# Kernel optimization log

Measured on AMD Instinct MI355X. Metric: run time of the kernel, lower is better.

## Reference

```python
import jax, jax.numpy as jnp
import numpy as np

B, S, H, NH, P = 1, 2048, 1024, 16, 2
D = H // NH
SCALE = 1.0 / np.sqrt(D).astype(np.float32)


def _lin(x, W, b):
    # x: [..., in] @ W: [in, out] + b: [out]
    return x @ W + b


def _split_heads(x):
    # [..., S, H] -> [..., NH, S, D]
    return x.reshape(*x.shape[:-2], x.shape[-2], NH, D).swapaxes(-3, -2)


def _merge_heads(x):
    # [..., NH, S, D] -> [..., S, H]
    return x.swapaxes(-3, -2).reshape(*x.shape[:-3], x.shape[-2], H)


def setup_inputs() -> dict:
    key = jax.random.key(0)
    ks = jax.random.split(key, 20)
    w = lambda k, i, o: jax.random.normal(k, (i, o), jnp.float32) * 0.02
    inp = {
        "hidden_states": jax.random.normal(ks[0], (B, S, H), jnp.float32),
        "past_states": jax.random.normal(ks[1], (P, B, S, H), jnp.float32),
        "Wq": w(ks[2], H, H), "bq": jnp.zeros((H,), jnp.float32),
        "Wk": w(ks[3], H, H), "bk": jnp.zeros((H,), jnp.float32),
        "Wv": w(ks[4], H, H), "bv": jnp.zeros((H,), jnp.float32),
        "Wo": w(ks[5], H, H), "bo": jnp.zeros((H,), jnp.float32),
        "Wrq": w(ks[6], H, H), "brq": jnp.zeros((H,), jnp.float32),
        "Wrk": w(ks[7], H, H), "brk": jnp.zeros((H,), jnp.float32),
        "Wrv": w(ks[8], H, H), "brv": jnp.zeros((H,), jnp.float32),
        "Wg": w(ks[9], 2 * H, H), "bg": jnp.zeros((H,), jnp.float32),
    }
    return inp


def reference(hidden_states, past_states, Wq, bq, Wk, bk, Wv, bv, Wo, bo,
              Wrq, brq, Wrk, brk, Wrv, brv, Wg, bg):
    # --- standard self-attention ---
    q = _split_heads(_lin(hidden_states, Wq, bq))  # [B,NH,S,D]
    k = _split_heads(_lin(hidden_states, Wk, bk))
    v = _split_heads(_lin(hidden_states, Wv, bv))
    scores = jnp.einsum('bhsd,bhtd->bhst', q, k) * SCALE
    attn = jax.nn.softmax(scores, axis=-1)
    ctx = jnp.einsum('bhst,bhtd->bhsd', attn, v)
    output = _lin(_merge_heads(ctx), Wo, bo)  # [B,S,H]

    # --- recursive attention over past states (recursion_level > 0) ---
    rq = _split_heads(_lin(output, Wrq, brq))           # [B,NH,S,D]
    rk = _split_heads(_lin(past_states, Wrk, brk))      # [P,B,NH,S,D]
    rv = _split_heads(_lin(past_states, Wrv, brv))
    rscores = jnp.einsum('bhsd,pbhtd->pbhst', rq, rk) * SCALE
    rattn = jax.nn.softmax(rscores, axis=-1)
    rctx = jnp.einsum('pbhst,pbhtd->pbhsd', rattn, rv)
    recursive_output = _merge_heads(rctx).mean(axis=0)  # [B,S,H]

    gate = jax.nn.sigmoid(_lin(jnp.concatenate([output, recursive_output], axis=-1), Wg, bg))
    output = output * (1.0 - gate) + recursive_output * gate
    return output
```

## Files before the change

### kernel.cpp

```cpp
#include <hip/hip_runtime.h>
#include <hip/hip_bf16.h>

#define S_LEN 2048
#define HDIM  1024
#define NHEAD 16
#define DHEAD 64
#define SCALE_F 0.125f
#define QSCALE  (0.125f * 1.44269504088896340736f)

typedef __bf16 bf16;
typedef __bf16 bf16x4 __attribute__((ext_vector_type(4)));
typedef __bf16 bf16x8 __attribute__((ext_vector_type(8)));
typedef float  f32x4  __attribute__((ext_vector_type(4)));

#define MFMA16(a,b,c) __builtin_amdgcn_mfma_f32_16x16x32_bf16((a),(b),(c),0,0,0)

__device__ __forceinline__ void gload16(const bf16* g, bf16* lds_wave_base) {
  __builtin_amdgcn_global_load_lds(
      (const __attribute__((address_space(1))) void*)g,
      (__attribute__((address_space(3))) void*)lds_wave_base, 16, 0, 0);
}

__global__ void cvt_f32_bf16_kernel(const float* __restrict__ in,
                                    bf16* __restrict__ out, int n4) {
  int i = blockIdx.x * blockDim.x + threadIdx.x;
  int stride = gridDim.x * blockDim.x;
  for (; i < n4; i += stride) {
    float4 v = ((const float4*)in)[i];
    bf16x4 o = { (bf16)v.x, (bf16)v.y, (bf16)v.z, (bf16)v.w };
    ((bf16x4*)out)[i] = o;
  }
}

struct TrJob { const float* in; bf16* out; };
struct TrArgs { TrJob j[8]; };

__global__ void transp_cvt_kernel(TrArgs args, int rows, int cols) {
  TrJob t = args.j[blockIdx.z];
  __shared__ float tile[32][33];
  int tx = threadIdx.x, ty = threadIdx.y;
  int c0 = blockIdx.x * 32, r0 = blockIdx.y * 32;
  for (int j = ty; j < 32; j += 8)
    tile[j][tx] = t.in[(size_t)(r0 + j) * cols + c0 + tx];
  __syncthreads();
  for (int j = ty; j < 32; j += 8)
    t.out[(size_t)(c0 + j) * rows + r0 + tx] = (bf16)tile[tx][j];
}

__global__ void transp_head_kernel(const bf16* __restrict__ in,
                                   bf16* __restrict__ out) {
  __shared__ bf16 tile[32][33];
  int h = blockIdx.z;
  int t0 = blockIdx.x * 32, d0 = blockIdx.y * 32;
  int tx = threadIdx.x, ty = threadIdx.y;
  for (int j = ty; j < 32; j += 8)
    tile[j][tx] = in[(size_t)(t0 + j) * HDIM + h * DHEAD + d0 + tx];
  __syncthreads();
  for (int j = ty; j < 32; j += 8)
    out[((size_t)h * DHEAD + d0 + j) * S_LEN + t0 + tx] = tile[tx][j];
}

struct GemmJob { const bf16* A; const bf16* Bt; const float* bias; bf16* Cb; float* Cf; float cscale; };
struct GemmArgs { GemmJob j[6]; };

__launch_bounds__(256)
__global__ void gemm_bt_kernel(GemmArgs args, int M, int N, int K) {
  GemmJob jb = args.j[blockIdx.z];
  const int bn = blockIdx.x, bm = blockIdx.y;
  const int tid = threadIdx.x;
  const int wave = tid >> 6, lane = tid & 63;
  const int wr = wave >> 1, wc = wave & 1;
  const int l16 = lane & 15, lq = lane >> 4;

  __shared__ alignas(16) bf16 As[128 * 32];
  __shared__ alignas(16) bf16 Bs[128 * 32];

  f32x4 acc[4][4];
#pragma unroll
  for (int i = 0; i < 4; ++i)
#pragma unroll
    for (int j = 0; j < 4; ++j) acc[i][j] = (f32x4){0.f, 0.f, 0.f, 0.f};

  const bf16* Ap = jb.A + (size_t)bm * 128 * K;
  const bf16* Bp = jb.Bt + (size_t)bn * 128 * K;

  const int r0 = tid >> 2,           c0 = (tid & 3) << 3;
  const int r1 = (tid + 256) >> 2,   c1 = ((tid + 256) & 3) << 3;
  bf16* ldsA0 = As + wave * 512;
  bf16* ldsA1 = As + 2048 + wave * 512;
  bf16* ldsB0 = Bs + wave * 512;
  bf16* ldsB1 = Bs + 2048 + wave * 512;

  for (int kt = 0; kt < K; kt += 32) {
    __syncthreads();
    gload16(Ap + (size_t)r0 * K + kt + c0, ldsA0);
    gload16(Ap + (size_t)r1 * K + kt + c1, ldsA1);
    gload16(Bp + (size_t)r0 * K + kt + c0, ldsB0);
    gload16(Bp + (size_t)r1 * K + kt + c1, ldsB1);
    __syncthreads();

    bf16x8 af[4], bfr[4];
#pragma unroll
    for (int i = 0; i < 4; ++i)
      af[i] = *(const bf16x8*)(As + (size_t)(wr * 64 + i * 16 + l16) * 32 + lq * 8);
#pragma unroll
    for (int j = 0; j < 4; ++j)
      bfr[j] = *(const bf16x8*)(Bs + (size_t)(wc * 64 + j * 16 + l16) * 32 + lq * 8);
#pragma unroll
    for (int i = 0; i < 4; ++i)
#pragma unroll
      for (int j = 0; j < 4; ++j)
        acc[i][j] = MFMA16(af[i], bfr[j], acc[i][j]);
  }

#pragma unroll
  for (int i = 0; i < 4; ++i) {
#pragma unroll
    for (int j = 0; j < 4; ++j) {
      int row0 = bm * 128 + wr * 64 + i * 16 + lq * 4;
      int col  = bn * 128 + wc * 64 + j * 16 + l16;
      float bv = jb.bias ? jb.bias[col] : 0.0f;
#pragma unroll
      for (int r = 0; r < 4; ++r) {
        float v = (acc[i][j][r] + bv) * jb.cscale;
        size_t off = (size_t)(row0 + r) * N + col;
        if (jb.Cb) jb.Cb[off] = (bf16)v;
        if (jb.Cf) jb.Cf[off] = v;
      }
    }
  }
}

__launch_bounds__(256)
__global__ void flash_attn_kernel(const bf16* __restrict__ Q,
                                  const bf16* __restrict__ Kin,
                                  const bf16* __restrict__ VT,
                                  bf16* __restrict__ Ob,
                                  float* __restrict__ Of,
                                  size_t kStride, size_t vStride, size_t oStride) {
  const int qb = blockIdx.x, h = blockIdx.y, p = blockIdx.z;
  const bf16* Kp = Kin + (size_t)p * kStride;
  const bf16* Vp = VT + (size_t)p * vStride;
  const int tid = threadIdx.x;
  const int wave = tid >> 6, lane = tid & 63;
  const int l16 = lane & 15, lq = lane >> 4;

  __shared__ alignas(16) bf16 Ks[64][72];
  __shared__ alignas(16) bf16 Vs[64][72];
  __shared__ alignas(16) bf16 Ps[4][16][72];

  bf16x8 qf[2];
  {
    const bf16* qptr = Q + (size_t)(qb * 64 + wave * 16 + l16) * HDIM + h * DHEAD + lq * 8;
    qf[0] = *(const bf16x8*)qptr;
    qf[1] = *(const bf16x8*)(qptr + 32);
  }

  float m_run = -1e30f, l_run = 0.f;
  f32x4 oacc[4];
#pragma unroll
  for (int j = 0; j < 4; ++j) oacc[j] = (f32x4){0.f, 0.f, 0.f, 0.f};

  for (int tb = 0; tb < S_LEN / 64; ++tb) {
    __syncthreads();
#pragma unroll
    for (int it = 0; it < 2; ++it) {
      int idx = tid + it * 256;
      int r = idx >> 3, c8 = (idx & 7) << 3;
      *(bf16x8*)(&Ks[r][c8]) = *(const bf16x8*)(Kp + (size_t)(tb * 64 + r) * HDIM + h * DHEAD + c8);
      *(bf16x8*)(&Vs[r][c8]) = *(const bf16x8*)(Vp + ((size_t)h * DHEAD + r) * S_LEN + tb * 64 + c8);
    }
    __syncthreads();

    f32x4 sf[4];
#pragma unroll
    for (int j = 0; j < 4; ++j) sf[j] = (f32x4){0.f, 0.f, 0.f, 0.f};
#pragma unroll
    for (int j = 0; j < 4; ++j)
#pragma unroll
      for (int kk = 0; kk < 2; ++kk) {
        bf16x8 kf = *(const bf16x8*)(&Ks[j * 16 + l16][kk * 32 + lq * 8]);
        sf[j] = MFMA16(kf, qf[kk], sf[j]);
      }

    float mx = -1e30f;
#pragma unroll
    for (int j = 0; j < 4; ++j)
#pragma unroll
      for (int r = 0; r < 4; ++r) mx = fmaxf(mx, sf[j][r]);
    mx = fmaxf(mx, __shfl_xor(mx, 16));
    mx = fmaxf(mx, __shfl_xor(mx, 32));

    float mnew = fmaxf(m_run, mx);
    float corr = exp2f(m_run - mnew);
    m_run = mnew;

    float rs = 0.f;
#pragma unroll
    for (int j = 0; j < 4; ++j)
#pragma unroll
      for (int r = 0; r < 4; ++r) {
        float pv = exp2f(sf[j][r] - mnew);
        sf[j][r] = pv;
        rs += pv;
      }
    rs += __shfl_xor(rs, 16);
    rs += __shfl_xor(rs, 32);
    l_run = l_run * corr + rs;
#pragma unroll
    for (int j = 0; j < 4; ++j) {
      oacc[j][0] *= corr; oacc[j][1] *= corr; oacc[j][2] *= corr; oacc[j][3] *= corr;
    }

#pragma unroll
    for (int j = 0; j < 4; ++j) {
      bf16x4 pk = { (bf16)sf[j][0], (bf16)sf[j][1], (bf16)sf[j][2], (bf16)sf[j][3] };
      *(bf16x4*)(&Ps[wave][l16][j * 16 + lq * 4]) = pk;
    }
    asm volatile("s_waitcnt lgkmcnt(0)" ::: "memory");

    bf16x8 pf[2];
    pf[0] = *(const bf16x8*)(&Ps[wave][l16][lq * 8]);
    pf[1] = *(const bf16x8*)(&Ps[wave][l16][32 + lq * 8]);
#pragma unroll
    for (int j = 0; j < 4; ++j)
#pragma unroll
      for (int kk = 0; kk < 2; ++kk) {
        bf16x8 vtf = *(const bf16x8*)(&Vs[j * 16 + l16][kk * 32 + lq * 8]);
        oacc[j] = MFMA16(vtf, pf[kk], oacc[j]);
      }
  }

  const float inv = 1.0f / l_run;
  const int q = qb * 64 + wave * 16 + l16;
#pragma unroll
  for (int j = 0; j < 4; ++j) {
    size_t off = (size_t)q * HDIM + h * DHEAD + j * 16 + lq * 4;
    float o0 = oacc[j][0] * inv, o1 = oacc[j][1] * inv,
          o2 = oacc[j][2] * inv, o3 = oacc[j][3] * inv;
    if (Ob) {
      bf16x4 ov = { (bf16)o0, (bf16)o1, (bf16)o2, (bf16)o3 };
      *(bf16x4*)(Ob + off) = ov;
    }
    if (Of) {
      float4 ov = { o0, o1, o2, o3 };
      *(float4*)(Of + (size_t)p * oStride + off) = ov;
    }
  }
}

__global__ void mean_gate_prep_kernel(const float* __restrict__ rc,
                                      const bf16* __restrict__ outb,
                                      float* __restrict__ rof,
                                      bf16* __restrict__ acat,
                                      int n) {
  int i = blockIdx.x * blockDim.x + threadIdx.x;
  int stride = gridDim.x * blockDim.x;
  for (; i < n; i += stride) {
    float ro = 0.5f * (rc[i] + rc[i + n]);
    rof[i] = ro;
    int srow = i >> 10, col = i & 1023;
    size_t base = (size_t)srow * 2048;
    acat[base + col] = outb[i];
    acat[base + 1024 + col] = (bf16)ro;
  }
}

__global__ void final_gate_kernel(const float* __restrict__ outf,
                                  const float* __restrict__ rof,
                                  const float* __restrict__ glog,
                                  float* __restrict__ out, int n) {
  int i = blockIdx.x * blockDim.x + threadIdx.x;
  int stride = gridDim.x * blockDim.x;
  for (; i < n; i += stride) {
    float g = 1.0f / (1.0f + __expf(-glog[i]));
    out[i] = outf[i] * (1.0f - g) + rof[i] * g;
  }
}

extern "C" void kernel_launch(void* const* d_in, const int* in_sizes, int n_in,
                              void* d_out, int out_size, void* d_ws, size_t ws_size,
                              hipStream_t stream) {
  const float* hs   = (const float*)d_in[0];
  const float* past = (const float*)d_in[1];
  const float* Wq = (const float*)d_in[2];   const float* bq = (const float*)d_in[3];
  const float* Wk = (const float*)d_in[4];   const float* bk = (const float*)d_in[5];
  const float* Wv = (const float*)d_in[6];   const float* bv = (const float*)d_in[7];
  const float* Wo = (const float*)d_in[8];   const float* bo = (const float*)d_in[9];
  const float* Wrq = (const float*)d_in[10]; const float* brq = (const float*)d_in[11];
  const float* Wrk = (const float*)d_in[12]; const float* brk = (const float*)d_in[13];
  const float* Wrv = (const float*)d_in[14]; const float* brv = (const float*)d_in[15];
  const float* Wg  = (const float*)d_in[16]; const float* bg  = (const float*)d_in[17];

  char* wp = (char*)d_ws;
  auto alloc = [&](size_t bytes) -> void* {
    void* p = (void*)wp;
    wp += (bytes + 255) & ~(size_t)255;
    return p;
  };
  const size_t NE = (size_t)S_LEN * HDIM;

  bf16* hs_b   = (bf16*)alloc(NE * 2);
  bf16* past_b = (bf16*)alloc(2 * NE * 2);
  bf16* Wqt  = (bf16*)alloc((size_t)HDIM * HDIM * 2);
  bf16* Wkt  = (bf16*)alloc((size_t)HDIM * HDIM * 2);
  bf16* Wvt  = (bf16*)alloc((size_t)HDIM * HDIM * 2);
  bf16* Wot  = (bf16*)alloc((size_t)HDIM * HDIM * 2);
  bf16* Wrqt = (bf16*)alloc((size_t)HDIM * HDIM * 2);
  bf16* Wrkt = (bf16*)alloc((size_t)HDIM * HDIM * 2);
  bf16* Wrvt = (bf16*)alloc((size_t)HDIM * HDIM * 2);
  bf16* Wgt  = (bf16*)alloc((size_t)2 * HDIM * HDIM * 2);
  bf16* q_b   = (bf16*)alloc(NE * 2);
  bf16* k_b   = (bf16*)alloc(NE * 2);
  bf16* v_b   = (bf16*)alloc(NE * 2);
  bf16* vT_b  = (bf16*)alloc(NE * 2);
  bf16* ctx_b = (bf16*)alloc(NE * 2);
  bf16* out_b = (bf16*)alloc(NE * 2);
  float* out_f = (float*)alloc(NE * 4);
  bf16* rq_b  = (bf16*)alloc(NE * 2);
  bf16* rk_b  = (bf16*)alloc(2 * NE * 2);
  bf16* rv_b  = (bf16*)alloc(2 * NE * 2);
  bf16* rvT_b = (bf16*)alloc(2 * NE * 2);
  float* rctx_f = (float*)alloc(2 * NE * 4);
  float* ro_f   = (float*)alloc(NE * 4);
  bf16* acat_b  = (bf16*)alloc(2 * NE * 2);
  float* glog_f = (float*)alloc(NE * 4);

  cvt_f32_bf16_kernel<<<2048, 256, 0, stream>>>(hs, hs_b, (int)(NE / 4));
  cvt_f32_bf16_kernel<<<2048, 256, 0, stream>>>(past, past_b, (int)(2 * NE / 4));

  TrArgs ta{};
  ta.j[0] = {Wq, Wqt};  ta.j[1] = {Wk, Wkt};  ta.j[2] = {Wv, Wvt};
  ta.j[3] = {Wo, Wot};  ta.j[4] = {Wrq, Wrqt}; ta.j[5] = {Wrk, Wrkt};
  ta.j[6] = {Wrv, Wrvt};
  transp_cvt_kernel<<<dim3(32, 32, 7), dim3(32, 8), 0, stream>>>(ta, 1024, 1024);
  TrArgs tg{};
  tg.j[0] = {Wg, Wgt};
  transp_cvt_kernel<<<dim3(32, 64, 1), dim3(32, 8), 0, stream>>>(tg, 2048, 1024);

  GemmArgs g1{};
  g1.j[0] = {hs_b, Wqt, bq, q_b, nullptr, QSCALE};
  g1.j[1] = {hs_b, Wkt, bk, k_b, nullptr, 1.0f};
  g1.j[2] = {hs_b, Wvt, bv, v_b, nullptr, 1.0f};
  gemm_bt_kernel<<<dim3(8, 16, 3), 256, 0, stream>>>(g1, 2048, 1024, 1024);

  transp_head_kernel<<<dim3(64, 2, 16), dim3(32, 8), 0, stream>>>(v_b, vT_b);

  flash_attn_kernel<<<dim3(32, 16, 1), 256, 0, stream>>>(
      q_b, k_b, vT_b, ctx_b, nullptr, 0, 0, 0);

  GemmArgs g2{};
  g2.j[0] = {ctx_b, Wot, bo, out_b, out_f, 1.0f};
  gemm_bt_kernel<<<dim3(8, 16, 1), 256, 0, stream>>>(g2, 2048, 1024, 1024);

  GemmArgs g3{};
  g3.j[0] = {out_b,        Wrqt, brq, rq_b,      nullptr, QSCALE};
  g3.j[1] = {past_b,       Wrkt, brk, rk_b,      nullptr, 1.0f};
  g3.j[2] = {past_b + NE,  Wrkt, brk, rk_b + NE, nullptr, 1.0f};
  g3.j[3] = {past_b,       Wrvt, brv, rv_b,      nullptr, 1.0f};
  g3.j[4] = {past_b + NE,  Wrvt, brv, rv_b + NE, nullptr, 1.0f};
  gemm_bt_kernel<<<dim3(8, 16, 5), 256, 0, stream>>>(g3, 2048, 1024, 1024);

  transp_head_kernel<<<dim3(64, 2, 16), dim3(32, 8), 0, stream>>>(rv_b, rvT_b);
  transp_head_kernel<<<dim3(64, 2, 16), dim3(32, 8), 0, stream>>>(rv_b + NE, rvT_b + NE);

  flash_attn_kernel<<<dim3(32, 16, 2), 256, 0, stream>>>(
      rq_b, rk_b, rvT_b, nullptr, rctx_f, NE, NE, NE);

  mean_gate_prep_kernel<<<2048, 256, 0, stream>>>(rctx_f, out_b, ro_f, acat_b, (int)NE);

  GemmArgs g4{};
  g4.j[0] = {acat_b, Wgt, bg, nullptr, glog_f, 1.0f};
  gemm_bt_kernel<<<dim3(8, 16, 1), 256, 0, stream>>>(g4, 2048, 1024, 2048);

  final_gate_kernel<<<2048, 256, 0, stream>>>(out_f, ro_f, glog_f, (float*)d_out, (int)NE);
}
```

Measured before the change: 474.6 us.

## Double-buffer GEMM and attention tiles, shrink GEMM M-tile, batch independent projections

Result: faster. 434.5 us (-8.4%).

```diff
diff --git a/kernel.cpp b/kernel.cpp
--- a/kernel.cpp
+++ b/kernel.cpp
@@ -5,7 +5,6 @@
 #define HDIM  1024
 #define NHEAD 16
 #define DHEAD 64
-#define SCALE_F 0.125f
 #define QSCALE  (0.125f * 1.44269504088896340736f)
 
 typedef __bf16 bf16;
@@ -47,21 +46,24 @@
     t.out[(size_t)(c0 + j) * rows + r0 + tx] = (bf16)tile[tx][j];
 }
 
-__global__ void transp_head_kernel(const bf16* __restrict__ in,
-                                   bf16* __restrict__ out) {
+struct ThJob { const bf16* in; bf16* out; };
+struct ThArgs { ThJob j[4]; };
+
+__global__ void transp_head_kernel(ThArgs args) {
+  ThJob t = args.j[blockIdx.z >> 4];
+  int h = blockIdx.z & 15;
   __shared__ bf16 tile[32][33];
-  int h = blockIdx.z;
   int t0 = blockIdx.x * 32, d0 = blockIdx.y * 32;
   int tx = threadIdx.x, ty = threadIdx.y;
   for (int j = ty; j < 32; j += 8)
-    tile[j][tx] = in[(size_t)(t0 + j) * HDIM + h * DHEAD + d0 + tx];
+    tile[j][tx] = t.in[(size_t)(t0 + j) * HDIM + h * DHEAD + d0 + tx];
   __syncthreads();
   for (int j = ty; j < 32; j += 8)
-    out[((size_t)h * DHEAD + d0 + j) * S_LEN + t0 + tx] = tile[tx][j];
+    t.out[((size_t)h * DHEAD + d0 + j) * S_LEN + t0 + tx] = tile[tx][j];
 }
 
 struct GemmJob { const bf16* A; const bf16* Bt; const float* bias; bf16* Cb; float* Cf; float cscale; };
-struct GemmArgs { GemmJob j[6]; };
+struct GemmArgs { GemmJob j[8]; };
 
 __launch_bounds__(256)
 __global__ void gemm_bt_kernel(GemmArgs args, int M, int N, int K) {
@@ -72,52 +74,57 @@
   const int wr = wave >> 1, wc = wave & 1;
   const int l16 = lane & 15, lq = lane >> 4;
 
-  __shared__ alignas(16) bf16 As[128 * 32];
-  __shared__ alignas(16) bf16 Bs[128 * 32];
-
-  f32x4 acc[4][4];
-#pragma unroll
-  for (int i = 0; i < 4; ++i)
+  __shared__ alignas(16) bf16 As[2][64 * 32];
+  __shared__ alignas(16) bf16 Bs[2][128 * 32];
+
+  f32x4 acc[2][4];
+#pragma unroll
+  for (int i = 0; i < 2; ++i)
 #pragma unroll
     for (int j = 0; j < 4; ++j) acc[i][j] = (f32x4){0.f, 0.f, 0.f, 0.f};
 
-  const bf16* Ap = jb.A + (size_t)bm * 128 * K;
+  const bf16* Ap = jb.A + (size_t)bm * 64 * K;
   const bf16* Bp = jb.Bt + (size_t)bn * 128 * K;
 
-  const int r0 = tid >> 2,           c0 = (tid & 3) << 3;
-  const int r1 = (tid + 256) >> 2,   c1 = ((tid + 256) & 3) << 3;
-  bf16* ldsA0 = As + wave * 512;
-  bf16* ldsA1 = As + 2048 + wave * 512;
-  bf16* ldsB0 = Bs + wave * 512;
-  bf16* ldsB1 = Bs + 2048 + wave * 512;
-
-  for (int kt = 0; kt < K; kt += 32) {
-    __syncthreads();
-    gload16(Ap + (size_t)r0 * K + kt + c0, ldsA0);
-    gload16(Ap + (size_t)r1 * K + kt + c1, ldsA1);
-    gload16(Bp + (size_t)r0 * K + kt + c0, ldsB0);
-    gload16(Bp + (size_t)r1 * K + kt + c1, ldsB1);
-    __syncthreads();
-
-    bf16x8 af[4], bfr[4];
-#pragma unroll
-    for (int i = 0; i < 4; ++i)
-      af[i] = *(const bf16x8*)(As + (size_t)(wr * 64 + i * 16 + l16) * 32 + lq * 8);
+  const int c0 = wave * 64 + lane;
+  const int r0 = c0 >> 2, c08 = (c0 & 3) << 3;
+
+  auto STAGE = [&](int buf, int kt) {
+    gload16(Ap + (size_t)r0 * K + kt + c08, &As[buf][wave * 512]);
+    gload16(Bp + (size_t)r0 * K + kt + c08, &Bs[buf][wave * 512]);
+    gload16(Bp + (size_t)(r0 + 64) * K + kt + c08, &Bs[buf][2048 + wave * 512]);
+  };
+
+  const int NT = K >> 5;
+  STAGE(0, 0);
+  __syncthreads();
+
+  for (int t = 0; t < NT; ++t) {
+    const int cur = t & 1;
+    const int ktn = (t + 1 < NT) ? (t + 1) * 32 : t * 32;
+    STAGE(cur ^ 1, ktn);
+
+    bf16x8 af[2], bfr[4];
+#pragma unroll
+    for (int i = 0; i < 2; ++i)
+      af[i] = *(const bf16x8*)(&As[cur][(wr * 32 + i * 16 + l16) * 32 + lq * 8]);
 #pragma unroll
     for (int j = 0; j < 4; ++j)
-      bfr[j] = *(const bf16x8*)(Bs + (size_t)(wc * 64 + j * 16 + l16) * 32 + lq * 8);
-#pragma unroll
-    for (int i = 0; i < 4; ++i)
+      bfr[j] = *(const bf16x8*)(&Bs[cur][(wc * 64 + j * 16 + l16) * 32 + lq * 8]);
+#pragma unroll
+    for (int i = 0; i < 2; ++i)
 #pragma unroll
       for (int j = 0; j < 4; ++j)
         acc[i][j] = MFMA16(af[i], bfr[j], acc[i][j]);
-  }
-
-#pragma unroll
-  for (int i = 0; i < 4; ++i) {
+
+    __syncthreads();
+  }
+
+#pragma unroll
+  for (int i = 0; i < 2; ++i) {
 #pragma unroll
     for (int j = 0; j < 4; ++j) {
-      int row0 = bm * 128 + wr * 64 + i * 16 + lq * 4;
+      int row0 = bm * 64 + wr * 32 + i * 16 + lq * 4;
       int col  = bn * 128 + wc * 64 + j * 16 + l16;
       float bv = jb.bias ? jb.bias[col] : 0.0f;
 #pragma unroll
@@ -145,9 +152,27 @@
   const int wave = tid >> 6, lane = tid & 63;
   const int l16 = lane & 15, lq = lane >> 4;
 
-  __shared__ alignas(16) bf16 Ks[64][72];
-  __shared__ alignas(16) bf16 Vs[64][72];
+  __shared__ alignas(16) bf16 Ks[2][64][72];
+  __shared__ alignas(16) bf16 Vs[2][64][72];
   __shared__ alignas(16) bf16 Ps[4][16][72];
+
+  const int i0 = tid, i1 = tid + 256;
+  const int ra = i0 >> 3, ca = (i0 & 7) << 3;
+  const int rb = i1 >> 3, cb = (i1 & 7) << 3;
+
+  bf16x8 krg[2], vrg[2];
+  auto LOAD_TILE = [&](int tb) {
+    krg[0] = *(const bf16x8*)(Kp + (size_t)(tb * 64 + ra) * HDIM + h * DHEAD + ca);
+    krg[1] = *(const bf16x8*)(Kp + (size_t)(tb * 64 + rb) * HDIM + h * DHEAD + cb);
+    vrg[0] = *(const bf16x8*)(Vp + ((size_t)h * DHEAD + ra) * S_LEN + tb * 64 + ca);
+    vrg[1] = *(const bf16x8*)(Vp + ((size_t)h * DHEAD + rb) * S_LEN + tb * 64 + cb);
+  };
+  auto STORE_TILE = [&](int buf) {
+    *(bf16x8*)(&Ks[buf][ra][ca]) = krg[0];
+    *(bf16x8*)(&Ks[buf][rb][cb]) = krg[1];
+    *(bf16x8*)(&Vs[buf][ra][ca]) = vrg[0];
+    *(bf16x8*)(&Vs[buf][rb][cb]) = vrg[1];
+  };
 
   bf16x8 qf[2];
   {
@@ -161,16 +186,15 @@
 #pragma unroll
   for (int j = 0; j < 4; ++j) oacc[j] = (f32x4){0.f, 0.f, 0.f, 0.f};
 
-  for (int tb = 0; tb < S_LEN / 64; ++tb) {
-    __syncthreads();
-#pragma unroll
-    for (int it = 0; it < 2; ++it) {
-      int idx = tid + it * 256;
-      int r = idx >> 3, c8 = (idx & 7) << 3;
-      *(bf16x8*)(&Ks[r][c8]) = *(const bf16x8*)(Kp + (size_t)(tb * 64 + r) * HDIM + h * DHEAD + c8);
-      *(bf16x8*)(&Vs[r][c8]) = *(const bf16x8*)(Vp + ((size_t)h * DHEAD + r) * S_LEN + tb * 64 + c8);
-    }
-    __syncthreads();
+  const int NT = S_LEN / 64;
+  LOAD_TILE(0);
+  STORE_TILE(0);
+  __syncthreads();
+
+  for (int tb = 0; tb < NT; ++tb) {
+    const int cur = tb & 1;
+    const bool more = (tb + 1 < NT);
+    if (more) LOAD_TILE(tb + 1);
 
     f32x4 sf[4];
 #pragma unroll
@@ -179,7 +203,7 @@
     for (int j = 0; j < 4; ++j)
 #pragma unroll
       for (int kk = 0; kk < 2; ++kk) {
-        bf16x8 kf = *(const bf16x8*)(&Ks[j * 16 + l16][kk * 32 + lq * 8]);
+        bf16x8 kf = *(const bf16x8*)(&Ks[cur][j * 16 + l16][kk * 32 + lq * 8]);
         sf[j] = MFMA16(kf, qf[kk], sf[j]);
       }
 
@@ -226,9 +250,14 @@
     for (int j = 0; j < 4; ++j)
 #pragma unroll
       for (int kk = 0; kk < 2; ++kk) {
-        bf16x8 vtf = *(const bf16x8*)(&Vs[j * 16 + l16][kk * 32 + lq * 8]);
+        bf16x8 vtf = *(const bf16x8*)(&Vs[cur][j * 16 + l16][kk * 32 + lq * 8]);
         oacc[j] = MFMA16(vtf, pf[kk], oacc[j]);
       }
+
+    if (more) {
+      STORE_TILE(cur ^ 1);
+      __syncthreads();
+    }
   }
 
   const float inv = 1.0f / l_run;
@@ -339,30 +368,31 @@
   transp_cvt_kernel<<<dim3(32, 64, 1), dim3(32, 8), 0, stream>>>(tg, 2048, 1024);
 
   GemmArgs g1{};
-  g1.j[0] = {hs_b, Wqt, bq, q_b, nullptr, QSCALE};
-  g1.j[1] = {hs_b, Wkt, bk, k_b, nullptr, 1.0f};
-  g1.j[2] = {hs_b, Wvt, bv, v_b, nullptr, 1.0f};
-  gemm_bt_kernel<<<dim3(8, 16, 3), 256, 0, stream>>>(g1, 2048, 1024, 1024);
-
-  transp_head_kernel<<<dim3(64, 2, 16), dim3(32, 8), 0, stream>>>(v_b, vT_b);
+  g1.j[0] = {hs_b,        Wqt,  bq,  q_b,        nullptr, QSCALE};
+  g1.j[1] = {hs_b,        Wkt,  bk,  k_b,        nullptr, 1.0f};
+  g1.j[2] = {hs_b,        Wvt,  bv,  v_b,        nullptr, 1.0f};
+  g1.j[3] = {past_b,      Wrkt, brk, rk_b,       nullptr, 1.0f};
+  g1.j[4] = {past_b + NE, Wrkt, brk, rk_b + NE,  nullptr, 1.0f};
+  g1.j[5] = {past_b,      Wrvt, brv, rv_b,       nullptr, 1.0f};
+  g1.j[6] = {past_b + NE, Wrvt, brv, rv_b + NE,  nullptr, 1.0f};
+  gemm_bt_kernel<<<dim3(8, 32, 7), 256, 0, stream>>>(g1, 2048, 1024, 1024);
+
+  ThArgs th{};
+  th.j[0] = {v_b, vT_b};
+  th.j[1] = {rv_b, rvT_b};
+  th.j[2] = {rv_b + NE, rvT_b + NE};
+  transp_head_kernel<<<dim3(64, 2, 48), dim3(32, 8), 0, stream>>>(th);
 
   flash_attn_kernel<<<dim3(32, 16, 1), 256, 0, stream>>>(
       q_b, k_b, vT_b, ctx_b, nullptr, 0, 0, 0);
 
   GemmArgs g2{};
   g2.j[0] = {ctx_b, Wot, bo, out_b, out_f, 1.0f};
-  gemm_bt_kernel<<<dim3(8, 16, 1), 256, 0, stream>>>(g2, 2048, 1024, 1024);
+  gemm_bt_kernel<<<dim3(8, 32, 1), 256, 0, stream>>>(g2, 2048, 1024, 1024);
 
   GemmArgs g3{};
-  g3.j[0] = {out_b,        Wrqt, brq, rq_b,      nullptr, QSCALE};
-  g3.j[1] = {past_b,       Wrkt, brk, rk_b,      nullptr, 1.0f};
-  g3.j[2] = {past_b + NE,  Wrkt, brk, rk_b + NE, nullptr, 1.0f};
-  g3.j[3] = {past_b,       Wrvt, brv, rv_b,      nullptr, 1.0f};
-  g3.j[4] = {past_b + NE,  Wrvt, brv, rv_b + NE, nullptr, 1.0f};
-  gemm_bt_kernel<<<dim3(8, 16, 5), 256, 0, stream>>>(g3, 2048, 1024, 1024);
-
-  transp_head_kernel<<<dim3(64, 2, 16), dim3(32, 8), 0, stream>>>(rv_b, rvT_b);
-  transp_head_kernel<<<dim3(64, 2, 16), dim3(32, 8), 0, stream>>>(rv_b + NE, rvT_b + NE);
+  g3.j[0] = {out_b, Wrqt, brq, rq_b, nullptr, QSCALE};
+  gemm_bt_kernel<<<dim3(8, 32, 1), 256, 0, stream>>>(g3, 2048, 1024, 1024);
 
   flash_attn_kernel<<<dim3(32, 16, 2), 256, 0, stream>>>(
       rq_b, rk_b, rvT_b, nullptr, rctx_f, NE, NE, NE);
@@ -371,7 +401,7 @@
 
   GemmArgs g4{};
   g4.j[0] = {acat_b, Wgt, bg, nullptr, glog_f, 1.0f};
-  gemm_bt_kernel<<<dim3(8, 16, 1), 256, 0, stream>>>(g4, 2048, 1024, 2048);
+  gemm_bt_kernel<<<dim3(8, 32, 1), 256, 0, stream>>>(g4, 2048, 1024, 2048);
 
   final_gate_kernel<<<2048, 256, 0, stream>>>(out_f, ro_f, glog_f, (float*)d_out, (int)NE);
 }
```
